# Optimization experiments

Measured on AMD Instinct MI355X. Metric: run time of the kernel, lower is better.

The kernel has to match this reference:

```python
import jax, jax.numpy as jnp
import numpy as np

DIM = 1024
K = 9            # kernel_size
PAD = 4          # padding = (K-1)//2


def setup_inputs() -> dict:
    key = jax.random.key(0)
    k1, k2, k3, k4, k5 = jax.random.split(key, 5)
    b, l, d = 4, 4096, DIM
    s = 1.0 / np.sqrt(d)
    x = jax.random.normal(k1, (b, l, d), dtype=jnp.float32)
    # linear2: dim -> k^2 + k   (torch Linear: y = x @ W.T + b)
    w2 = jax.random.uniform(k2, (K * K + K, d), jnp.float32, -s, s)
    b2 = jax.random.uniform(k3, (K * K + K,), jnp.float32, -s, s)
    # outlinear: dim -> dim
    wo = jax.random.uniform(k4, (d, d), jnp.float32, -s, s)
    bo = jax.random.uniform(k5, (d,), jnp.float32, -s, s)
    return {"x": x, "w2": w2, "b2": b2, "wo": wo, "bo": bo}


def reference(x, w2, b2, wo, bo):
    b, l, d = x.shape
    # per-token generated weights / bias
    att = x @ w2.T + b2                                  # (b, l, k^2 + k)
    aw = jnp.sin(att[..., : K * K]).reshape(b, l, K, K)  # (b, l, k, k)
    ab = att[..., K * K :]                               # (b, l, k)
    # sliding windows along sequence: (b, l, d, k)
    xp = jnp.pad(x, ((0, 0), (PAD, PAD), (0, 0)))
    windows = jnp.stack([xp[:, i : i + l] for i in range(K)], axis=-1)
    # sum_j (windows @ aw)[..., j] == windows @ aw.sum(-1); bias sums over k, broadcast over d
    y = jnp.einsum("bldk,blk->bld", windows, aw.sum(axis=-1)) + ab.sum(axis=-1, keepdims=True)
    return y @ wo.T + bo
```

## Files before the change

kernel.cpp:

```cpp
#include <hip/hip_runtime.h>
#include <hip/hip_bf16.h>

#define DIM   1024
#define SEQL  4096
#define NTOK  16384
#define NATT  90
#define NATTP 96

typedef __attribute__((ext_vector_type(8))) short frag_ab;
typedef __attribute__((ext_vector_type(4))) float frag_cd;

typedef unsigned int u32;
typedef const __attribute__((address_space(1))) u32* gp_t;
typedef __attribute__((address_space(3))) u32* lp_t;

static __device__ __forceinline__ unsigned short f2bf(float f) {
    unsigned int u = __float_as_uint(f);
    return (unsigned short)((u + 0x7fffu + ((u >> 16) & 1u)) >> 16);
}
static __device__ __forceinline__ ushort4 f4tobf(float4 v) {
    ushort4 r; r.x = f2bf(v.x); r.y = f2bf(v.y); r.z = f2bf(v.z); r.w = f2bf(v.w);
    return r;
}

__global__ __launch_bounds__(256) void cvt_kernel(
    const float* __restrict__ w2, const float* __restrict__ wo,
    unsigned short* __restrict__ w2p, unsigned short* __restrict__ wob)
{
    const int bid = blockIdx.x;
    if (bid < 1024) {
        const int i = bid * 256 + threadIdx.x;
        float4 v = ((const float4*)wo)[i];
        *(ushort4*)(wob + (size_t)i * 4) = f4tobf(v);
    } else {
        const int idx = (bid - 1024) * 256 + threadIdx.x;
        const int c    = idx / 384;
        const int rem  = idx - c * 384;
        const int f    = rem >> 6;
        const int lane = rem & 63;
        const int row  = f * 16 + (lane & 15);
        const int col  = c * 32 + (lane >> 4) * 8;
        float4 v0 = make_float4(0.f, 0.f, 0.f, 0.f), v1 = v0;
        if (row < NATT) {
            v0 = *(const float4*)(w2 + (size_t)row * DIM + col);
            v1 = *(const float4*)(w2 + (size_t)row * DIM + col + 4);
        }
        unsigned short* dst = w2p + (size_t)idx * 8;
        *(ushort4*)(dst)     = f4tobf(v0);
        *(ushort4*)(dst + 4) = f4tobf(v1);
    }
}

#define ATOK 16
#define PSTR 98

__global__ __launch_bounds__(256) void att_coeff_kernel(
    const float* __restrict__ x, const unsigned short* __restrict__ w2p,
    const float* __restrict__ b2, float* __restrict__ cws)
{
    __shared__ __align__(16) char shbuf[ATOK * 1024 * 2];
    __shared__ float summ[ATOK * NATTP];
    __shared__ float b2s[NATTP];

    unsigned short* xs   = (unsigned short*)shbuf;
    float*          part = (float*)shbuf;

    const int tid  = threadIdx.x;
    const int wave = tid >> 6, lane = tid & 63;
    const int fr = lane & 15, kq = lane >> 4;
    const int tok0 = blockIdx.x * ATOK;

    if (tid < NATTP) b2s[tid] = (tid < NATT) ? b2[tid] : 0.f;

    #pragma unroll
    for (int t = 0; t < 4; ++t) {
        const int row = t * 4 + wave;
        const float4* xr = (const float4*)(x + (size_t)(tok0 + row) * DIM);
        #pragma unroll
        for (int tt = 0; tt < 4; ++tt) {
            const int c4 = tt * 64 + lane;
            float4 v = xr[c4];
            const int ch = c4 >> 1, half = c4 & 1;
            *(ushort4*)(&xs[row * 1024 + ((ch ^ (row & 7)) * 8 + half * 4)]) = f4tobf(v);
        }
    }
    __syncthreads();

    frag_cd acc[6] = {};
    #pragma unroll
    for (int kk = 0; kk < 8; ++kk) {
        const int ch = wave * 32 + kk * 4 + kq;
        frag_ab a = *(const frag_ab*)(&xs[fr * 1024 + ((ch ^ (fr & 7)) * 8)]);
        const int c = wave * 8 + kk;
        #pragma unroll
        for (int f = 0; f < 6; ++f) {
            frag_ab b = *(const frag_ab*)(w2p + ((size_t)((c * 6 + f) * 64) + lane) * 8);
            acc[f] = __builtin_amdgcn_mfma_f32_16x16x32_bf16(a, b, acc[f], 0, 0, 0);
        }
    }
    __syncthreads();

    const int col = lane & 15, rb = (lane >> 4) * 4;
    #pragma unroll
    for (int f = 0; f < 6; ++f)
        #pragma unroll
        for (int r = 0; r < 4; ++r)
            part[(wave * 16 + rb + r) * PSTR + f * 16 + col] = acc[f][r];
    __syncthreads();

    for (int o = tid; o < ATOK * NATTP; o += 256) {
        const int t = o / NATTP, m = o - (o / NATTP) * NATTP;
        float s = b2s[m];
        #pragma unroll
        for (int w = 0; w < 4; ++w) s += part[(w * 16 + t) * PSTR + m];
        summ[t * NATTP + m] = s;
    }
    __syncthreads();

    if (tid < 160) {
        const int t = tid / 10, j = tid - (tid / 10) * 10;
        float s = 0.f;
        if (j < 9) {
            #pragma unroll
            for (int jj = 0; jj < 9; ++jj) s += sinf(summ[t * NATTP + j * 9 + jj]);
        } else {
            #pragma unroll
            for (int m = NATT - 9; m < NATT; ++m) s += summ[t * NATTP + m];
        }
        cws[(size_t)(tok0 + t) * 10 + j] = s;
    }
}

#define TT 32

__global__ __launch_bounds__(256) void y_kernel(
    const float* __restrict__ x, const float* __restrict__ cws,
    unsigned short* __restrict__ ybf)
{
    __shared__ float c[TT][10];
    const int tid  = threadIdx.x;
    const int tok0 = blockIdx.x * TT;

    for (int i = tid; i < TT * 10; i += 256)
        c[i / 10][i % 10] = cws[(size_t)tok0 * 10 + i];
    __syncthreads();

    const int b  = tok0 >> 12;
    const int l0 = tok0 & 4095;
    const float4* xv = (const float4*)x + (size_t)b * SEQL * (DIM / 4) + tid;
    const float4 z4 = make_float4(0.f, 0.f, 0.f, 0.f);

    float4 w[9];
    #pragma unroll
    for (int k = 0; k < 8; ++k) {
        const int src = l0 + k - 4;
        w[k] = (src >= 0 && src < SEQL) ? xv[(size_t)src * (DIM / 4)] : z4;
    }

    ushort4* yp = (ushort4*)(ybf + (size_t)tok0 * DIM + tid * 4);

    #pragma unroll
    for (int t = 0; t < TT; ++t) {
        const int src = l0 + t + 4;
        w[8] = (src < SEQL) ? xv[(size_t)src * (DIM / 4)] : z4;

        float4 acc;
        acc.x = acc.y = acc.z = acc.w = c[t][9];
        #pragma unroll
        for (int k = 0; k < 9; ++k) {
            const float ck = c[t][k];
            acc.x += ck * w[k].x; acc.y += ck * w[k].y;
            acc.z += ck * w[k].z; acc.w += ck * w[k].w;
        }
        yp[(size_t)t * (DIM / 4)] = f4tobf(acc);

        #pragma unroll
        for (int k = 0; k < 8; ++k) w[k] = w[k + 1];
    }
}

#define GBM 256
#define GBN 256
#define GBK 64

#define STAGE(d, kt)                                                           \
    {                                                                          \
        const int kc_ = (kt) * GBK;                                            \
        _Pragma("unroll")                                                      \
        for (int j_ = 0; j_ < 4; ++j_) {                                       \
            __builtin_amdgcn_global_load_lds(                                  \
                (gp_t)(A + (size_t)(m0 + srow[j_]) * DIM + kc_ + scol[j_]),    \
                (lp_t)(&As[d][(wave * 4 + j_) * 512]), 16, 0, 0);              \
            __builtin_amdgcn_global_load_lds(                                  \
                (gp_t)(Bm + (size_t)(n0 + srow[j_]) * DIM + kc_ + scol[j_]),   \
                (lp_t)(&Bs[d][(wave * 4 + j_) * 512]), 16, 0, 0);              \
        }                                                                      \
    }

__global__ __launch_bounds__(512, 2) void gemm_kernel(
    const unsigned short* __restrict__ A,
    const unsigned short* __restrict__ Bm,
    const float* __restrict__ bo,
    float* __restrict__ out)
{
    __shared__ unsigned short As[2][GBM * GBK];
    __shared__ unsigned short Bs[2][GBN * GBK];

    const int tid  = threadIdx.x;
    const int wave = tid >> 6, lane = tid & 63;
    const int fr = lane & 15, kq = lane >> 4;
    const int wm = (wave >> 2) * 128;
    const int wn = (wave & 3) * 64;

    const int bid = blockIdx.x;
    const int lid = (bid & 7) * 32 + (bid >> 3);
    const int m0  = (lid >> 2) * GBM;
    const int n0  = (lid & 3) * GBN;

    int srow[4], scol[4];
    #pragma unroll
    for (int j = 0; j < 4; ++j) {
        int ci = (wave * 4 + j) * 64 + lane;
        int row = ci >> 3;
        srow[j] = row;
        scol[j] = ((ci & 7) ^ (row & 7)) * 8;
    }

    frag_cd acc[8][4] = {};

    STAGE(0, 0);
    STAGE(1, 1);

    for (int kt = 0; kt < 15; ++kt) {
        const int d = kt & 1;
        asm volatile("s_waitcnt vmcnt(8)" ::: "memory");
        __builtin_amdgcn_s_barrier();

        frag_ab b0[4], b1[4];
        #pragma unroll
        for (int ni = 0; ni < 4; ++ni) {
            int row = wn + ni * 16 + fr;
            b0[ni] = *(const frag_ab*)(&Bs[d][row * 64 + ((kq       ^ (row & 7)) * 8)]);
            b1[ni] = *(const frag_ab*)(&Bs[d][row * 64 + (((4 + kq) ^ (row & 7)) * 8)]);
        }
        frag_ab alo0[4], alo1[4];
        #pragma unroll
        for (int mi = 0; mi < 4; ++mi) {
            int row = wm + mi * 16 + fr;
            alo0[mi] = *(const frag_ab*)(&As[d][row * 64 + ((kq       ^ (row & 7)) * 8)]);
            alo1[mi] = *(const frag_ab*)(&As[d][row * 64 + (((4 + kq) ^ (row & 7)) * 8)]);
        }
        __builtin_amdgcn_s_setprio(1);
        #pragma unroll
        for (int mi = 0; mi < 4; ++mi)
            #pragma unroll
            for (int ni = 0; ni < 4; ++ni) {
                acc[mi][ni] = __builtin_amdgcn_mfma_f32_16x16x32_bf16(alo0[mi], b0[ni], acc[mi][ni], 0, 0, 0);
                acc[mi][ni] = __builtin_amdgcn_mfma_f32_16x16x32_bf16(alo1[mi], b1[ni], acc[mi][ni], 0, 0, 0);
            }
        __builtin_amdgcn_s_setprio(0);
        frag_ab ahi0[4], ahi1[4];
        #pragma unroll
        for (int mi = 0; mi < 4; ++mi) {
            int row = wm + (mi + 4) * 16 + fr;
            ahi0[mi] = *(const frag_ab*)(&As[d][row * 64 + ((kq       ^ (row & 7)) * 8)]);
            ahi1[mi] = *(const frag_ab*)(&As[d][row * 64 + (((4 + kq) ^ (row & 7)) * 8)]);
        }
        asm volatile("s_waitcnt lgkmcnt(0)" ::: "memory");
        __builtin_amdgcn_s_barrier();
        if (kt < 14) { STAGE(d, kt + 2); }
        __builtin_amdgcn_s_setprio(1);
        #pragma unroll
        for (int mi = 0; mi < 4; ++mi)
            #pragma unroll
            for (int ni = 0; ni < 4; ++ni) {
                acc[mi + 4][ni] = __builtin_amdgcn_mfma_f32_16x16x32_bf16(ahi0[mi], b0[ni], acc[mi + 4][ni], 0, 0, 0);
                acc[mi + 4][ni] = __builtin_amdgcn_mfma_f32_16x16x32_bf16(ahi1[mi], b1[ni], acc[mi + 4][ni], 0, 0, 0);
            }
        __builtin_amdgcn_s_setprio(0);
    }

    {
        asm volatile("s_waitcnt vmcnt(0)" ::: "memory");
        __builtin_amdgcn_s_barrier();
        frag_ab b0[4], b1[4];
        #pragma unroll
        for (int ni = 0; ni < 4; ++ni) {
            int row = wn + ni * 16 + fr;
            b0[ni] = *(const frag_ab*)(&Bs[1][row * 64 + ((kq       ^ (row & 7)) * 8)]);
            b1[ni] = *(const frag_ab*)(&Bs[1][row * 64 + (((4 + kq) ^ (row & 7)) * 8)]);
        }
        #pragma unroll
        for (int h = 0; h < 2; ++h) {
            frag_ab a0[4], a1[4];
            #pragma unroll
            for (int mi = 0; mi < 4; ++mi) {
                int row = wm + (mi + h * 4) * 16 + fr;
                a0[mi] = *(const frag_ab*)(&As[1][row * 64 + ((kq       ^ (row & 7)) * 8)]);
                a1[mi] = *(const frag_ab*)(&As[1][row * 64 + (((4 + kq) ^ (row & 7)) * 8)]);
            }
            __builtin_amdgcn_s_setprio(1);
            #pragma unroll
            for (int mi = 0; mi < 4; ++mi)
                #pragma unroll
                for (int ni = 0; ni < 4; ++ni) {
                    acc[mi + h * 4][ni] = __builtin_amdgcn_mfma_f32_16x16x32_bf16(a0[mi], b0[ni], acc[mi + h * 4][ni], 0, 0, 0);
                    acc[mi + h * 4][ni] = __builtin_amdgcn_mfma_f32_16x16x32_bf16(a1[mi], b1[ni], acc[mi + h * 4][ni], 0, 0, 0);
                }
            __builtin_amdgcn_s_setprio(0);
        }
    }

    const int colb = lane & 15, rb = (lane >> 4) * 4;
    #pragma unroll
    for (int ni = 0; ni < 4; ++ni) {
        const int col = n0 + wn + ni * 16 + colb;
        const float bias = bo[col];
        #pragma unroll
        for (int mi = 0; mi < 8; ++mi) {
            #pragma unroll
            for (int r = 0; r < 4; ++r) {
                const int row = m0 + wm + mi * 16 + rb + r;
                out[(size_t)row * DIM + col] = acc[mi][ni][r] + bias;
            }
        }
    }
}

extern "C" void kernel_launch(void* const* d_in, const int* in_sizes, int n_in,
                              void* d_out, int out_size, void* d_ws, size_t ws_size,
                              hipStream_t stream) {
    const float* x  = (const float*)d_in[0];
    const float* w2 = (const float*)d_in[1];
    const float* b2 = (const float*)d_in[2];
    const float* wo = (const float*)d_in[3];
    const float* bo = (const float*)d_in[4];
    float* out = (float*)d_out;

    char* ws = (char*)d_ws;
    float*          cws = (float*)ws;
    unsigned short* wob = (unsigned short*)(ws + 655360);
    unsigned short* ybf = (unsigned short*)(ws + 655360 + 2097152);
    unsigned short* w2p = (unsigned short*)(ws + 655360 + 2097152 + 33554432);

    cvt_kernel<<<1024 + 48, 256, 0, stream>>>(w2, wo, w2p, wob);
    att_coeff_kernel<<<NTOK / ATOK, 256, 0, stream>>>(x, w2p, b2, cws);
    y_kernel<<<NTOK / TT, 256, 0, stream>>>(x, cws, ybf);
    gemm_kernel<<<NTOK / GBM * (DIM / GBN), 512, 0, stream>>>(ybf, wob, bo, out);
}
```

Before: 87.64 us.

## Fuse attention-coefficient and sliding-window y computation into one kernel

Merges the coefficient kernel and the y kernel so each block computes its 16 tokens' coefficients and then immediately forms y from the bf16 copy of x already held in LDS, loading only an 8-row halo from global memory. This removes a full second pass over x (64 MB fp32) and one kernel launch. The in-LDS partial-sum reduction now uses two buffers plus an accumulate step instead of a four-way sum. In exchange, the window inputs are now bf16-rounded copies of x rather than fp32, which slightly changes numerics, and LDS use grows.

```diff
diff --git a/kernel.cpp b/kernel.cpp
--- a/kernel.cpp
+++ b/kernel.cpp
@@ -20,6 +20,14 @@
 }
 static __device__ __forceinline__ ushort4 f4tobf(float4 v) {
     ushort4 r; r.x = f2bf(v.x); r.y = f2bf(v.y); r.z = f2bf(v.z); r.w = f2bf(v.w);
+    return r;
+}
+static __device__ __forceinline__ float4 bf4tof(ushort4 u) {
+    float4 r;
+    r.x = __uint_as_float((u32)u.x << 16);
+    r.y = __uint_as_float((u32)u.y << 16);
+    r.z = __uint_as_float((u32)u.z << 16);
+    r.w = __uint_as_float((u32)u.w << 16);
     return r;
 }
 
@@ -54,21 +62,22 @@
 #define ATOK 16
 #define PSTR 98
 
-__global__ __launch_bounds__(256) void att_coeff_kernel(
+__global__ __launch_bounds__(256) void att_y_kernel(
     const float* __restrict__ x, const unsigned short* __restrict__ w2p,
-    const float* __restrict__ b2, float* __restrict__ cws)
+    const float* __restrict__ b2, unsigned short* __restrict__ ybf)
 {
-    __shared__ __align__(16) char shbuf[ATOK * 1024 * 2];
+    __shared__ __align__(16) unsigned short xs[ATOK * 1024];
+    __shared__ float part[2 * ATOK * PSTR];
     __shared__ float summ[ATOK * NATTP];
     __shared__ float b2s[NATTP];
-
-    unsigned short* xs   = (unsigned short*)shbuf;
-    float*          part = (float*)shbuf;
+    __shared__ float coe[ATOK][12];
 
     const int tid  = threadIdx.x;
     const int wave = tid >> 6, lane = tid & 63;
     const int fr = lane & 15, kq = lane >> 4;
     const int tok0 = blockIdx.x * ATOK;
+    const int bb = tok0 >> 12;
+    const int l0 = tok0 & 4095;
 
     if (tid < NATTP) b2s[tid] = (tid < NATT) ? b2[tid] : 0.f;
 
@@ -84,6 +93,17 @@
             *(ushort4*)(&xs[row * 1024 + ((ch ^ (row & 7)) * 8 + half * 4)]) = f4tobf(v);
         }
     }
+
+    const float4 z4 = make_float4(0.f, 0.f, 0.f, 0.f);
+    float4 halo[8];
+    #pragma unroll
+    for (int hh = 0; hh < 8; ++hh) {
+        const int off = (hh < 4) ? (hh - 4) : (hh + 12);
+        const int src = l0 + off;
+        halo[hh] = z4;
+        if (src >= 0 && src < SEQL)
+            halo[hh] = *((const float4*)(x + ((size_t)bb * SEQL + src) * DIM) + tid);
+    }
     __syncthreads();
 
     frag_cd acc[6] = {};
@@ -98,22 +118,29 @@
             acc[f] = __builtin_amdgcn_mfma_f32_16x16x32_bf16(a, b, acc[f], 0, 0, 0);
         }
     }
-    __syncthreads();
 
     const int col = lane & 15, rb = (lane >> 4) * 4;
-    #pragma unroll
-    for (int f = 0; f < 6; ++f)
-        #pragma unroll
-        for (int r = 0; r < 4; ++r)
-            part[(wave * 16 + rb + r) * PSTR + f * 16 + col] = acc[f][r];
+    float* myp = &part[(wave & 1) * ATOK * PSTR];
+    if (wave < 2) {
+        #pragma unroll
+        for (int f = 0; f < 6; ++f)
+            #pragma unroll
+            for (int r = 0; r < 4; ++r)
+                myp[(rb + r) * PSTR + f * 16 + col] = acc[f][r];
+    }
+    __syncthreads();
+    if (wave >= 2) {
+        #pragma unroll
+        for (int f = 0; f < 6; ++f)
+            #pragma unroll
+            for (int r = 0; r < 4; ++r)
+                myp[(rb + r) * PSTR + f * 16 + col] += acc[f][r];
+    }
     __syncthreads();
 
     for (int o = tid; o < ATOK * NATTP; o += 256) {
         const int t = o / NATTP, m = o - (o / NATTP) * NATTP;
-        float s = b2s[m];
-        #pragma unroll
-        for (int w = 0; w < 4; ++w) s += part[(w * 16 + t) * PSTR + m];
-        summ[t * NATTP + m] = s;
+        summ[o] = b2s[m] + part[t * PSTR + m] + part[ATOK * PSTR + t * PSTR + m];
     }
     __syncthreads();
 
@@ -127,53 +154,34 @@
             #pragma unroll
             for (int m = NATT - 9; m < NATT; ++m) s += summ[t * NATTP + m];
         }
-        cws[(size_t)(tok0 + t) * 10 + j] = s;
-    }
-}
-
-#define TT 32
-
-__global__ __launch_bounds__(256) void y_kernel(
-    const float* __restrict__ x, const float* __restrict__ cws,
-    unsigned short* __restrict__ ybf)
-{
-    __shared__ float c[TT][10];
-    const int tid  = threadIdx.x;
-    const int tok0 = blockIdx.x * TT;
-
-    for (int i = tid; i < TT * 10; i += 256)
-        c[i / 10][i % 10] = cws[(size_t)tok0 * 10 + i];
-    __syncthreads();
-
-    const int b  = tok0 >> 12;
-    const int l0 = tok0 & 4095;
-    const float4* xv = (const float4*)x + (size_t)b * SEQL * (DIM / 4) + tid;
-    const float4 z4 = make_float4(0.f, 0.f, 0.f, 0.f);
+        coe[t][j] = s;
+    }
+    __syncthreads();
+
+    const int ch2 = tid >> 1, hf2 = tid & 1;
+    auto rowval = [&](int rel) -> float4 {
+        if (rel < 0)  return halo[rel + 4];
+        if (rel > 15) return halo[rel - 12];
+        ushort4 u = *(const ushort4*)(&xs[rel * 1024 + ((ch2 ^ (rel & 7)) * 8 + hf2 * 4)]);
+        return bf4tof(u);
+    };
 
     float4 w[9];
     #pragma unroll
-    for (int k = 0; k < 8; ++k) {
-        const int src = l0 + k - 4;
-        w[k] = (src >= 0 && src < SEQL) ? xv[(size_t)src * (DIM / 4)] : z4;
-    }
-
-    ushort4* yp = (ushort4*)(ybf + (size_t)tok0 * DIM + tid * 4);
-
-    #pragma unroll
-    for (int t = 0; t < TT; ++t) {
-        const int src = l0 + t + 4;
-        w[8] = (src < SEQL) ? xv[(size_t)src * (DIM / 4)] : z4;
-
-        float4 acc;
-        acc.x = acc.y = acc.z = acc.w = c[t][9];
+    for (int k = 0; k < 8; ++k) w[k] = rowval(k - 4);
+
+    #pragma unroll
+    for (int t = 0; t < ATOK; ++t) {
+        w[8] = rowval(t + 4);
+        float4 a4;
+        a4.x = a4.y = a4.z = a4.w = coe[t][9];
         #pragma unroll
         for (int k = 0; k < 9; ++k) {
-            const float ck = c[t][k];
-            acc.x += ck * w[k].x; acc.y += ck * w[k].y;
-            acc.z += ck * w[k].z; acc.w += ck * w[k].w;
-        }
-        yp[(size_t)t * (DIM / 4)] = f4tobf(acc);
-
+            const float ck = coe[t][k];
+            a4.x += ck * w[k].x; a4.y += ck * w[k].y;
+            a4.z += ck * w[k].z; a4.w += ck * w[k].w;
+        }
+        *(ushort4*)(ybf + (size_t)(tok0 + t) * DIM + tid * 4) = f4tobf(a4);
         #pragma unroll
         for (int k = 0; k < 8; ++k) w[k] = w[k + 1];
     }
@@ -338,13 +346,11 @@
     float* out = (float*)d_out;
 
     char* ws = (char*)d_ws;
-    float*          cws = (float*)ws;
-    unsigned short* wob = (unsigned short*)(ws + 655360);
-    unsigned short* ybf = (unsigned short*)(ws + 655360 + 2097152);
-    unsigned short* w2p = (unsigned short*)(ws + 655360 + 2097152 + 33554432);
+    unsigned short* wob = (unsigned short*)ws;
+    unsigned short* ybf = (unsigned short*)(ws + 2097152);
+    unsigned short* w2p = (unsigned short*)(ws + 2097152 + 33554432);
 
     cvt_kernel<<<1024 + 48, 256, 0, stream>>>(w2, wo, w2p, wob);
-    att_coeff_kernel<<<NTOK / ATOK, 256, 0, stream>>>(x, w2p, b2, cws);
-    y_kernel<<<NTOK / TT, 256, 0, stream>>>(x, cws, ybf);
+    att_y_kernel<<<NTOK / ATOK, 256, 0, stream>>>(x, w2p, b2, ybf);
     gemm_kernel<<<NTOK / GBM * (DIM / GBN), 512, 0, stream>>>(ybf, wob, bo, out);
 }
```

Result: faster. 77.80 us (-11.2%).
